# Optimization experiments

Measured on AMD Instinct MI355X. Metric: run time of the kernel, lower is better.

## Reference

```python
import jax, jax.numpy as jnp
import numpy as np

N = 50000        # nodes
E = 800000       # random edges (plus N self-loops added in setup)
DIN = 128        # input_dim
H = 128          # hidden_dim
L = 3            # num_layers
EPS = 1e-5       # BatchNorm1d eps


def _bn(x, gamma, beta):
    # BatchNorm1d in training mode: batch stats over node axis, biased variance
    m = x.mean(axis=0)
    v = jnp.mean((x - m) ** 2, axis=0)
    return (x - m) * jax.lax.rsqrt(v + EPS) * gamma + beta


def setup_inputs() -> dict:
    key = jax.random.key(0)
    ks = jax.random.split(key, 11)
    feats = jax.random.normal(ks[0], (N, DIN), dtype=jnp.float32)
    # edge list with self-loops so every node has degree >= 1 (average pooling divides by degree)
    loops = jnp.arange(N, dtype=jnp.int64)
    src = jnp.concatenate([jax.random.randint(ks[1], (E,), 0, N, dtype=jnp.int64), loops])
    dst = jnp.concatenate([jax.random.randint(ks[2], (E,), 0, N, dtype=jnp.int64), loops])
    s = 0.05
    # per-layer MLP params (num_mlp_layers=2: Linear -> BN -> ReLU -> Linear), layer 0 has DIN==H
    W1 = jax.random.normal(ks[3], (L, DIN, H), dtype=jnp.float32) * s
    b1 = jnp.zeros((L, H), jnp.float32)
    g1 = jnp.ones((L, H), jnp.float32)
    be1 = jnp.zeros((L, H), jnp.float32)
    W2 = jax.random.normal(ks[4], (L, H, H), dtype=jnp.float32) * s
    b2 = jnp.zeros((L, H), jnp.float32)
    # outer BatchNorm1d per GNN layer
    og = jnp.ones((L, H), jnp.float32)
    ob = jnp.zeros((L, H), jnp.float32)
    return {"feats": feats, "W1": W1, "b1": b1, "g1": g1, "be1": be1,
            "W2": W2, "b2": b2, "og": og, "ob": ob, "src": src, "dst": dst}


def reference(feats, W1, b1, g1, be1, W2, b2, og, ob, src, dst):
    n = feats.shape[0]
    # degree = spmm(Adj, ones) -- constant across layers
    deg = jax.ops.segment_sum(jnp.ones(src.shape, jnp.float32), dst, num_segments=n)[:, None]
    h = feats
    for l in range(L):
        # pooled = spmm(Adj, h) via edge gather + segment reduce, then 'average' normalize
        pooled = jax.ops.segment_sum(h[src], dst, num_segments=n) / deg
        # GIN-style 2-layer MLP: Linear -> BN -> ReLU -> Linear
        z = jax.nn.relu(_bn(pooled @ W1[l] + b1[l], g1[l], be1[l]))
        z = z @ W2[l] + b2[l]
        # outer BatchNorm + ReLU
        h = jax.nn.relu(_bn(z, og[l], ob[l]))
    return h
```

## Files before the change

### kernel.cpp

```cpp
#include <hip/hip_runtime.h>
#include <hip/hip_bf16.h>
#include <stdint.h>

typedef __hip_bfloat16 bf16;
typedef short bf16x8 __attribute__((ext_vector_type(8)));
typedef float f32x4 __attribute__((ext_vector_type(4)));

#define HF 128
#define EPS 1e-5f
#define BSH 9
#define BROWS 512
#define ECHUNK 8192

static __device__ __forceinline__ uint32_t pack_bf16(float a, float b) {
    union { bf16 h; unsigned short u; } ca, cb;
    ca.h = __float2bfloat16(a);
    cb.h = __float2bfloat16(b);
    return (uint32_t)ca.u | ((uint32_t)cb.u << 16);
}


__global__ __launch_bounds__(256) void k_bcount(const int* __restrict__ dst,
                                                int* __restrict__ bcnt, int ne, int nb) {
    __shared__ int h[128];
    const int tid = threadIdx.x;
    if (tid < nb) h[tid] = 0;
    __syncthreads();
    const int beg = blockIdx.x * ECHUNK;
    const int end = min(beg + ECHUNK, ne);
    for (int i = beg + tid; i < end; i += 256)
        atomicAdd(&h[dst[i] >> BSH], 1);
    __syncthreads();
    if (tid < nb && h[tid]) atomicAdd(&bcnt[tid], h[tid]);
}

__global__ __launch_bounds__(128) void k_bscan(const int* __restrict__ bcnt,
                                               int* __restrict__ bstart,
                                               int* __restrict__ gcursor,
                                               int* __restrict__ rowptr,
                                               int nb, int n, int ne) {
    if (threadIdx.x == 0) {
        int acc = 0;
        for (int b = 0; b < nb; b++) {
            bstart[b] = acc;
            gcursor[b] = acc;
            acc += bcnt[b];
        }
        bstart[nb] = acc;
        rowptr[n] = ne;
    }
}

__global__ __launch_bounds__(256) void k_bscatter(const int* __restrict__ src,
                                                  const int* __restrict__ dst,
                                                  int* __restrict__ gcursor,
                                                  int2* __restrict__ staging, int ne, int nb) {
    __shared__ int h[128], gb[128];
    const int tid = threadIdx.x;
    if (tid < nb) h[tid] = 0;
    __syncthreads();
    const int beg = blockIdx.x * ECHUNK;
    const int end = min(beg + ECHUNK, ne);
    for (int i = beg + tid; i < end; i += 256)
        atomicAdd(&h[dst[i] >> BSH], 1);
    __syncthreads();
    if (tid < nb) {
        int c = h[tid];
        gb[tid] = c ? atomicAdd(&gcursor[tid], c) : 0;
        h[tid] = 0;
    }
    __syncthreads();
    for (int i = beg + tid; i < end; i += 256) {
        int d = dst[i];
        int b = d >> BSH;
        int r = atomicAdd(&h[b], 1);
        staging[(size_t)gb[b] + r] = make_int2(src[i], d);
    }
}

__global__ __launch_bounds__(256) void k_bbuild(const int2* __restrict__ staging,
                                                const int* __restrict__ bstart,
                                                int* __restrict__ rowptr,
                                                float* __restrict__ deginv,
                                                int* __restrict__ csrsrc, int n) {
    __shared__ int hist[BROWS];
    __shared__ int scan[BROWS];
    const int b = blockIdx.x;
    const int tid = threadIdx.x;
    const int rb = b << BSH;
    const int nrows = min(BROWS, n - rb);
    const int ebeg = bstart[b], eend = bstart[b + 1];
    hist[tid] = 0; hist[tid + 256] = 0;
    __syncthreads();
    for (int i = ebeg + tid; i < eend; i += 256)
        atomicAdd(&hist[staging[i].y - rb], 1);
    __syncthreads();
    const int i0 = tid, i1 = tid + 256;
    scan[i0] = hist[i0]; scan[i1] = hist[i1];
    __syncthreads();
    for (int off = 1; off < BROWS; off <<= 1) {
        int v0 = (i0 >= off) ? scan[i0 - off] : 0;
        int v1 = (i1 >= off) ? scan[i1 - off] : 0;
        __syncthreads();
        scan[i0] += v0; scan[i1] += v1;
        __syncthreads();
    }
    for (int r = tid; r < BROWS; r += 256) {
        int c = hist[r];
        int excl = scan[r] - c;
        if (r < nrows) {
            rowptr[rb + r] = ebeg + excl;
            deginv[rb + r] = c ? 1.0f / (float)c : 0.f;
        }
        scan[r] = excl;
    }
    __syncthreads();
    for (int i = ebeg + tid; i < eend; i += 256) {
        int2 e = staging[i];
        int pos = atomicAdd(&scan[e.y - rb], 1);
        csrsrc[ebeg + pos] = e.x;
    }
}

__global__ __launch_bounds__(256) void k_wprep(const float* __restrict__ W1,
                                               const float* __restrict__ W2,
                                               bf16* __restrict__ wp) {
    const int mat = blockIdx.x >> 6;
    const int idx = ((blockIdx.x & 63) << 8) + threadIdx.x;
    const int l = mat >> 1;
    const float* Wsrc = (mat & 1) ? (W2 + l * 16384) : (W1 + l * 16384);
    const int nn = idx >> 7, k = idx & 127;
    float w = Wsrc[k * 128 + nn];
    int pos = nn * 128 + ((((k >> 3) ^ (nn & 7))) << 3) + (k & 7);
    wp[mat * 16384 + pos] = __float2bfloat16(w);
}

__global__ __launch_bounds__(256) void k_cvt(const float* __restrict__ in,
                                             uint32_t* __restrict__ out, long tot2) {
    long i = (long)blockIdx.x * 256 + threadIdx.x;
    if (i >= tot2) return;
    float2 v = ((const float2*)in)[i];
    out[i] = pack_bf16(v.x, v.y);
}

template <int AFF>
__global__ __launch_bounds__(256) void k_spmm(const uint32_t* __restrict__ hp,
                                              const int* __restrict__ rowptr,
                                              const int* __restrict__ csrsrc,
                                              const float* __restrict__ deginv,
                                              const float* __restrict__ st,
                                              const float* __restrict__ g,
                                              const float* __restrict__ be,
                                              float inv_n,
                                              uint32_t* __restrict__ pooled, int n, int np) {
    const int wid  = (int)((blockIdx.x * 256u + threadIdx.x) >> 6);
    const int lane = threadIdx.x & 63;
    if (wid >= np) return;
    uint32_t* outp = pooled + (size_t)wid * 64 + lane;
    if (wid >= n) { *outp = 0u; return; }
    float sx = 1.f, cx = 0.f, sy = 1.f, cy = 0.f;
    if (AFF) {
        const int c0 = lane * 2, c1 = c0 + 1;
        float m0 = st[c0] * inv_n, v0 = st[128 + c0] * inv_n - m0 * m0;
        sx = g[c0] * rsqrtf(v0 + EPS); cx = be[c0] - m0 * sx;
        float m1 = st[c1] * inv_n, v1 = st[128 + c1] * inv_n - m1 * m1;
        sy = g[c1] * rsqrtf(v1 + EPS); cy = be[c1] - m1 * sy;
    }
    float a0 = 0.f, a1 = 0.f;
    const int beg = rowptr[wid], end = rowptr[wid + 1];
    for (int base = beg; base < end; base += 64) {
        const int rem = end - base;
        const int cnt = rem < 64 ? rem : 64;
        const int off = lane < cnt ? lane : cnt - 1;
        const int idx = csrsrc[base + off];
        int j = 0;
        for (; j + 8 <= cnt; j += 8) {
            uint32_t p[8];
#pragma unroll
            for (int u = 0; u < 8; u++) {
                int s = __builtin_amdgcn_readlane(idx, j + u);
                p[u] = hp[(size_t)s * 64 + lane];
            }
#pragma unroll
            for (int u = 0; u < 8; u++) {
                float vx = __uint_as_float(p[u] << 16);
                float vy = __uint_as_float(p[u] & 0xFFFF0000u);
                if (AFF) {
                    vx = fmaxf(fmaf(vx, sx, cx), 0.f);
                    vy = fmaxf(fmaf(vy, sy, cy), 0.f);
                }
                a0 += vx; a1 += vy;
            }
        }
        for (; j < cnt; j++) {
            int s = __builtin_amdgcn_readlane(idx, j);
            uint32_t pk = hp[(size_t)s * 64 + lane];
            float vx = __uint_as_float(pk << 16);
            float vy = __uint_as_float(pk & 0xFFFF0000u);
            if (AFF) {
                vx = fmaxf(fmaf(vx, sx, cx), 0.f);
                vy = fmaxf(fmaf(vy, sy, cy), 0.f);
            }
            a0 += vx; a1 += vy;
        }
    }
    const float di = deginv[wid];
    *outp = pack_bf16(a0 * di, a1 * di);
}

template <int MODE, int OUTBF>
__global__ __launch_bounds__(256) void k_gemm(const bf16* __restrict__ Abf,
                                              const float* __restrict__ Af,
                                              const bf16* __restrict__ Wp,
                                              const float* __restrict__ bias,
                                              const float* __restrict__ st,
                                              const float* __restrict__ g,
                                              const float* __restrict__ be,
                                              float inv_n,
                                              float* __restrict__ Yf,
                                              bf16* __restrict__ Yb,
                                              float* __restrict__ outstats, int n) {
    __shared__ __align__(16) bf16 WT[128 * 128];
    __shared__ float sred[4][128];
    __shared__ float sred2[4][128];
    __shared__ float aff[256];
    const int tid = threadIdx.x;
    const int wave = tid >> 6, lane = tid & 63;

    {
        const char* gsrc = (const char*)Wp + wave * 1024 + lane * 16;
        char* ldst = (char*)&WT[0] + wave * 1024;
#pragma unroll
        for (int i = 0; i < 8; i++) {
            __builtin_amdgcn_global_load_lds(
                (const __attribute__((address_space(1))) uint32_t*)(gsrc + i * 4096),
                (__attribute__((address_space(3))) uint32_t*)(ldst + i * 4096),
                16, 0, 0);
        }
    }
    if (MODE == 1 && tid < 128) {
        float m = st[tid] * inv_n;
        float v = st[128 + tid] * inv_n - m * m;
        float a = g[tid] * rsqrtf(v + EPS);
        aff[tid] = a;
        aff[128 + tid] = be[tid] - m * a;
    }

    const int lrow = lane & 15, quad = lane >> 4;
    const int bx = (int)blockIdx.x * 128;
    int mb[2];
    mb[0] = bx + wave * 16;
    mb[1] = bx + 64 + wave * 16;

    bf16x8 ah[2][4], al[2][4];
    if (MODE == 0) {
#pragma unroll
        for (int rt = 0; rt < 2; rt++) {
            const bf16* arow = Abf + (size_t)(mb[rt] + lrow) * 128 + quad * 8;
#pragma unroll
            for (int kt = 0; kt < 4; kt++)
                ah[rt][kt] = *(const bf16x8*)(arow + kt * 32);
        }
    }

    __syncthreads();

    if (MODE == 1) {
#pragma unroll
        for (int rt = 0; rt < 2; rt++) {
            const float* arow = Af + (size_t)(mb[rt] + lrow) * 128 + quad * 8;
#pragma unroll
            for (int kt = 0; kt < 4; kt++) {
                short th[8], tl[8];
#pragma unroll
                for (int j = 0; j < 8; j++) {
                    int k = kt * 32 + quad * 8 + j;
                    float x = fmaxf(fmaf(arow[kt * 32 + j], aff[k], aff[128 + k]), 0.f);
                    union { bf16 b; short s; } ch, cl;
                    ch.b = __float2bfloat16(x);
                    cl.b = __float2bfloat16(x - __bfloat162float(ch.b));
                    th[j] = ch.s; tl[j] = cl.s;
                }
                ah[rt][kt] = *(bf16x8*)th;
                al[rt][kt] = *(bf16x8*)tl;
            }
        }
    }

    f32x4 acc[2][8];
#pragma unroll
    for (int rt = 0; rt < 2; rt++)
#pragma unroll
        for (int nt = 0; nt < 8; nt++) acc[rt][nt] = (f32x4){0.f, 0.f, 0.f, 0.f};

    const int sw = lrow & 7;
#pragma unroll
    for (int nt = 0; nt < 8; nt++) {
        const bf16* wbase = &WT[(nt * 16 + lrow) * 128];
#pragma unroll
        for (int kt = 0; kt < 4; kt++) {
            bf16x8 bh = *(const bf16x8*)(wbase + (((4 * kt + quad) ^ sw) << 3));
#pragma unroll
            for (int rt = 0; rt < 2; rt++) {
                acc[rt][nt] = __builtin_amdgcn_mfma_f32_16x16x32_bf16(ah[rt][kt], bh, acc[rt][nt], 0, 0, 0);
                if (MODE == 1)
                    acc[rt][nt] = __builtin_amdgcn_mfma_f32_16x16x32_bf16(al[rt][kt], bh, acc[rt][nt], 0, 0, 0);
            }
        }
    }

#pragma unroll
    for (int nt = 0; nt < 8; nt++) {
        int col = nt * 16 + lrow;
        float bv = bias[col];
        float csum = 0.f, csq = 0.f;
#pragma unroll
        for (int rt = 0; rt < 2; rt++) {
#pragma unroll
            for (int r = 0; r < 4; r++) {
                int row = mb[rt] + quad * 4 + r;
                float yv = acc[rt][nt][r] + bv;
                if (OUTBF) Yb[(size_t)row * 128 + col] = __float2bfloat16(yv);
                else       Yf[(size_t)row * 128 + col] = yv;
                if (row < n) { csum += yv; csq += yv * yv; }
            }
        }
        csum += __shfl_xor(csum, 16, 64); csum += __shfl_xor(csum, 32, 64);
        csq  += __shfl_xor(csq,  16, 64); csq  += __shfl_xor(csq,  32, 64);
        if (quad == 0) { sred[wave][col] = csum; sred2[wave][col] = csq; }
    }
    __syncthreads();
    if (tid < 128) {
        float s = sred[0][tid] + sred[1][tid] + sred[2][tid] + sred[3][tid];
        float q = sred2[0][tid] + sred2[1][tid] + sred2[2][tid] + sred2[3][tid];
        atomicAdd(&outstats[tid], s);
        atomicAdd(&outstats[128 + tid], q);
    }
}

__global__ __launch_bounds__(256) void k_bnrelu(const uint32_t* __restrict__ Z,
                                                const float* __restrict__ st,
                                                const float* __restrict__ g,
                                                const float* __restrict__ be,
                                                float inv_n,
                                                float* __restrict__ out, long tot2) {
    long i = (long)blockIdx.x * 256 + threadIdx.x;
    if (i >= tot2) return;
    int c = (int)((i * 2) & 127);
    float m0 = st[c] * inv_n,     v0 = st[128 + c] * inv_n - m0 * m0;
    float a0 = g[c] * rsqrtf(v0 + EPS),     c0 = be[c] - m0 * a0;
    float m1 = st[c + 1] * inv_n, v1 = st[129 + c] * inv_n - m1 * m1;
    float a1 = g[c + 1] * rsqrtf(v1 + EPS), c1 = be[c + 1] - m1 * a1;
    uint32_t pk = Z[i];
    float vx = __uint_as_float(pk << 16);
    float vy = __uint_as_float(pk & 0xFFFF0000u);
    float2 o;
    o.x = fmaxf(fmaf(vx, a0, c0), 0.f);
    o.y = fmaxf(fmaf(vy, a1, c1), 0.f);
    ((float2*)out)[i] = o;
}

extern "C" void kernel_launch(void* const* d_in, const int* in_sizes, int n_in,
                              void* d_out, int out_size, void* d_ws, size_t ws_size,
                              hipStream_t stream) {
    const float* feats = (const float*)d_in[0];
    const float* W1    = (const float*)d_in[1];
    const float* b1    = (const float*)d_in[2];
    const float* g1    = (const float*)d_in[3];
    const float* be1   = (const float*)d_in[4];
    const float* W2    = (const float*)d_in[5];
    const float* b2    = (const float*)d_in[6];
    const float* og    = (const float*)d_in[7];
    const float* ob    = (const float*)d_in[8];
    const int*   src   = (const int*)d_in[9];
    const int*   dst   = (const int*)d_in[10];

    const int n  = in_sizes[0] / HF;
    const int ne = in_sizes[9];
    const int np = (n + 127) & ~127;
    const int nb = (n + BROWS - 1) >> BSH;

    char* p = (char*)d_ws;
    auto alloc = [&](size_t bytes) -> char* {
        char* r = p;
        p += (bytes + 511) & ~(size_t)511;
        return r;
    };
    uint32_t* hbuf    = (uint32_t*)alloc((size_t)np * 64 * 4);
    uint32_t* pooled  = (uint32_t*)alloc((size_t)np * 64 * 4);
    float*    ybuf    = (float*)   alloc((size_t)np * HF * 4);
    uint32_t* zb      = (uint32_t*)alloc((size_t)np * 64 * 4);
    bf16*     wprep   = (bf16*)    alloc(6 * 16384 * 2);
    float*    deginv  = (float*)   alloc((size_t)n * 4);
    int*      rowptr  = (int*)     alloc((size_t)(n + 1) * 4);
    int*      csrsrc  = (int*)     alloc((size_t)ne * 4);
    int2*     staging = (int2*)    alloc((size_t)ne * 8);
    int*      bstart  = (int*)     alloc((size_t)(nb + 1) * 4);
    int*      gcursor = (int*)     alloc((size_t)nb * 4);
    char*     zone    = alloc(512 + 6 * 256 * 4);
    int*      bcnt    = (int*)zone;
    float*    stats6  = (float*)(zone + 512);

    hipMemsetAsync(zone, 0, 512 + 6 * 256 * 4, stream);

    const int ebk = (ne + ECHUNK - 1) / ECHUNK;
    k_wprep   <<<384, 256, 0, stream>>>(W1, W2, wprep);
    k_bcount  <<<ebk, 256, 0, stream>>>(dst, bcnt, ne, nb);
    k_bscan   <<<1, 128, 0, stream>>>(bcnt, bstart, gcursor, rowptr, nb, n, ne);
    k_bscatter<<<ebk, 256, 0, stream>>>(src, dst, gcursor, staging, ne, nb);
    k_bbuild  <<<nb, 256, 0, stream>>>(staging, bstart, rowptr, deginv, csrsrc, n);

    const long tot2  = (long)n * (HF / 2);
    const int bnb    = (int)((tot2 + 255) / 256);
    const int spmmb  = np / 4;
    const int gemmb  = np / 128;
    const float inv_n = 1.0f / (float)n;

    k_cvt<<<bnb, 256, 0, stream>>>(feats, hbuf, tot2);

    for (int l = 0; l < 3; l++) {
        float* sY = stats6 + (2 * l) * 256;
        float* sZ = stats6 + (2 * l + 1) * 256;
        if (l == 0)
            k_spmm<0><<<spmmb, 256, 0, stream>>>(hbuf, rowptr, csrsrc, deginv,
                                                 nullptr, nullptr, nullptr, inv_n,
                                                 pooled, n, np);
        else
            k_spmm<1><<<spmmb, 256, 0, stream>>>(zb, rowptr, csrsrc, deginv,
                                                 stats6 + (2 * (l - 1) + 1) * 256,
                                                 og + (l - 1) * HF, ob + (l - 1) * HF, inv_n,
                                                 pooled, n, np);
        k_gemm<0, 0><<<gemmb, 256, 0, stream>>>((const bf16*)pooled, nullptr,
                                                wprep + (size_t)(2 * l) * 16384,
                                                b1 + l * HF,
                                                nullptr, nullptr, nullptr, inv_n,
                                                ybuf, nullptr, sY, n);
        k_gemm<1, 1><<<gemmb, 256, 0, stream>>>(nullptr, ybuf,
                                                wprep + (size_t)(2 * l + 1) * 16384,
                                                b2 + l * HF,
                                                sY, g1 + l * HF, be1 + l * HF, inv_n,
                                                nullptr, (bf16*)zb, sZ, n);
    }
    k_bnrelu<<<bnb, 256, 0, stream>>>(zb, stats6 + 5 * 256, og + 2 * HF, ob + 2 * HF,
                                      inv_n, (float*)d_out, tot2);
}
```

Before: 395.0 us.

## Use fixed-capacity edge buckets, merge prep kernels, and bank BN stat atomics

```diff
diff --git a/kernel.cpp b/kernel.cpp
--- a/kernel.cpp
+++ b/kernel.cpp
@@ -10,7 +10,9 @@
 #define EPS 1e-5f
 #define BSH 9
 #define BROWS 512
+#define BCAP 16384
 #define ECHUNK 8192
+#define SBANKS 8
 
 static __device__ __forceinline__ uint32_t pack_bf16(float a, float b) {
     union { bf16 h; unsigned short u; } ca, cb;
@@ -19,37 +21,13 @@
     return (uint32_t)ca.u | ((uint32_t)cb.u << 16);
 }
 
-
-__global__ __launch_bounds__(256) void k_bcount(const int* __restrict__ dst,
-                                                int* __restrict__ bcnt, int ne, int nb) {
-    __shared__ int h[128];
-    const int tid = threadIdx.x;
-    if (tid < nb) h[tid] = 0;
-    __syncthreads();
-    const int beg = blockIdx.x * ECHUNK;
-    const int end = min(beg + ECHUNK, ne);
-    for (int i = beg + tid; i < end; i += 256)
-        atomicAdd(&h[dst[i] >> BSH], 1);
-    __syncthreads();
-    if (tid < nb && h[tid]) atomicAdd(&bcnt[tid], h[tid]);
-}
-
-__global__ __launch_bounds__(128) void k_bscan(const int* __restrict__ bcnt,
-                                               int* __restrict__ bstart,
-                                               int* __restrict__ gcursor,
-                                               int* __restrict__ rowptr,
-                                               int nb, int n, int ne) {
-    if (threadIdx.x == 0) {
-        int acc = 0;
-        for (int b = 0; b < nb; b++) {
-            bstart[b] = acc;
-            gcursor[b] = acc;
-            acc += bcnt[b];
-        }
-        bstart[nb] = acc;
-        rowptr[n] = ne;
-    }
-}
+static __device__ __forceinline__ float sum8(const float* __restrict__ st, int idx) {
+    float s = 0.f;
+#pragma unroll
+    for (int b = 0; b < SBANKS; b++) s += st[b * 256 + idx];
+    return s;
+}
+
 
 __global__ __launch_bounds__(256) void k_bscatter(const int* __restrict__ src,
                                                   const int* __restrict__ dst,
@@ -74,13 +52,14 @@
         int d = dst[i];
         int b = d >> BSH;
         int r = atomicAdd(&h[b], 1);
-        staging[(size_t)gb[b] + r] = make_int2(src[i], d);
+        staging[(size_t)b * BCAP + gb[b] + r] = make_int2(src[i], d);
     }
 }
 
 __global__ __launch_bounds__(256) void k_bbuild(const int2* __restrict__ staging,
-                                                const int* __restrict__ bstart,
-                                                int* __restrict__ rowptr,
+                                                const int* __restrict__ gcursor,
+                                                int* __restrict__ rowbeg,
+                                                int* __restrict__ rowend,
                                                 float* __restrict__ deginv,
                                                 int* __restrict__ csrsrc, int n) {
     __shared__ int hist[BROWS];
@@ -89,11 +68,12 @@
     const int tid = threadIdx.x;
     const int rb = b << BSH;
     const int nrows = min(BROWS, n - rb);
-    const int ebeg = bstart[b], eend = bstart[b + 1];
+    const int base = b * BCAP;
+    const int cnt = gcursor[b];
     hist[tid] = 0; hist[tid + 256] = 0;
     __syncthreads();
-    for (int i = ebeg + tid; i < eend; i += 256)
-        atomicAdd(&hist[staging[i].y - rb], 1);
+    for (int i = tid; i < cnt; i += 256)
+        atomicAdd(&hist[staging[base + i].y - rb], 1);
     __syncthreads();
     const int i0 = tid, i1 = tid + 256;
     scan[i0] = hist[i0]; scan[i1] = hist[i1];
@@ -109,49 +89,54 @@
         int c = hist[r];
         int excl = scan[r] - c;
         if (r < nrows) {
-            rowptr[rb + r] = ebeg + excl;
+            rowbeg[rb + r] = base + excl;
+            rowend[rb + r] = base + excl + c;
             deginv[rb + r] = c ? 1.0f / (float)c : 0.f;
         }
         scan[r] = excl;
     }
     __syncthreads();
-    for (int i = ebeg + tid; i < eend; i += 256) {
-        int2 e = staging[i];
+    for (int i = tid; i < cnt; i += 256) {
+        int2 e = staging[base + i];
         int pos = atomicAdd(&scan[e.y - rb], 1);
-        csrsrc[ebeg + pos] = e.x;
-    }
-}
-
-__global__ __launch_bounds__(256) void k_wprep(const float* __restrict__ W1,
-                                               const float* __restrict__ W2,
-                                               bf16* __restrict__ wp) {
-    const int mat = blockIdx.x >> 6;
-    const int idx = ((blockIdx.x & 63) << 8) + threadIdx.x;
-    const int l = mat >> 1;
-    const float* Wsrc = (mat & 1) ? (W2 + l * 16384) : (W1 + l * 16384);
-    const int nn = idx >> 7, k = idx & 127;
-    float w = Wsrc[k * 128 + nn];
-    int pos = nn * 128 + ((((k >> 3) ^ (nn & 7))) << 3) + (k & 7);
-    wp[mat * 16384 + pos] = __float2bfloat16(w);
-}
-
-__global__ __launch_bounds__(256) void k_cvt(const float* __restrict__ in,
-                                             uint32_t* __restrict__ out, long tot2) {
-    long i = (long)blockIdx.x * 256 + threadIdx.x;
-    if (i >= tot2) return;
-    float2 v = ((const float2*)in)[i];
-    out[i] = pack_bf16(v.x, v.y);
+        csrsrc[base + pos] = e.x;
+    }
+}
+
+__global__ __launch_bounds__(256) void k_prep(const float* __restrict__ W1,
+                                              const float* __restrict__ W2,
+                                              bf16* __restrict__ wp,
+                                              const float* __restrict__ feats,
+                                              uint32_t* __restrict__ hbuf, long tot2) {
+    const int bid = (int)blockIdx.x;
+    if (bid < 384) {
+        const int mat = bid >> 6;
+        const int idx = ((bid & 63) << 8) + (int)threadIdx.x;
+        const int l = mat >> 1;
+        const float* Wsrc = (mat & 1) ? (W2 + l * 16384) : (W1 + l * 16384);
+        const int nn = idx >> 7, k = idx & 127;
+        float w = Wsrc[k * 128 + nn];
+        int pos = nn * 128 + ((((k >> 3) ^ (nn & 7))) << 3) + (k & 7);
+        wp[mat * 16384 + pos] = __float2bfloat16(w);
+    } else {
+        long i = (long)(bid - 384) * 256 + threadIdx.x;
+        if (i < tot2) {
+            float2 v = ((const float2*)feats)[i];
+            hbuf[i] = pack_bf16(v.x, v.y);
+        }
+    }
 }
 
 template <int AFF>
 __global__ __launch_bounds__(256) void k_spmm(const uint32_t* __restrict__ hp,
-                                              const int* __restrict__ rowptr,
-                                              const int* __restrict__ csrsrc,
+                                              const int* __restrict__ rowbeg,
+                                              const int* __restrict__ rowend,
                                               const float* __restrict__ deginv,
                                               const float* __restrict__ st,
                                               const float* __restrict__ g,
                                               const float* __restrict__ be,
                                               float inv_n,
+                                              const int* __restrict__ csrsrc,
                                               uint32_t* __restrict__ pooled, int n, int np) {
     const int wid  = (int)((blockIdx.x * 256u + threadIdx.x) >> 6);
     const int lane = threadIdx.x & 63;
@@ -161,13 +146,13 @@
     float sx = 1.f, cx = 0.f, sy = 1.f, cy = 0.f;
     if (AFF) {
         const int c0 = lane * 2, c1 = c0 + 1;
-        float m0 = st[c0] * inv_n, v0 = st[128 + c0] * inv_n - m0 * m0;
+        float m0 = sum8(st, c0) * inv_n, v0 = sum8(st, 128 + c0) * inv_n - m0 * m0;
         sx = g[c0] * rsqrtf(v0 + EPS); cx = be[c0] - m0 * sx;
-        float m1 = st[c1] * inv_n, v1 = st[128 + c1] * inv_n - m1 * m1;
+        float m1 = sum8(st, c1) * inv_n, v1 = sum8(st, 128 + c1) * inv_n - m1 * m1;
         sy = g[c1] * rsqrtf(v1 + EPS); cy = be[c1] - m1 * sy;
     }
     float a0 = 0.f, a1 = 0.f;
-    const int beg = rowptr[wid], end = rowptr[wid + 1];
+    const int beg = rowbeg[wid], end = rowend[wid];
     for (int base = beg; base < end; base += 64) {
         const int rem = end - base;
         const int cnt = rem < 64 ? rem : 64;
@@ -239,8 +224,8 @@
         }
     }
     if (MODE == 1 && tid < 128) {
-        float m = st[tid] * inv_n;
-        float v = st[128 + tid] * inv_n - m * m;
+        float m = sum8(st, tid) * inv_n;
+        float v = sum8(st, 128 + tid) * inv_n - m * m;
         float a = g[tid] * rsqrtf(v + EPS);
         aff[tid] = a;
         aff[128 + tid] = be[tid] - m * a;
@@ -333,8 +318,9 @@
     if (tid < 128) {
         float s = sred[0][tid] + sred[1][tid] + sred[2][tid] + sred[3][tid];
         float q = sred2[0][tid] + sred2[1][tid] + sred2[2][tid] + sred2[3][tid];
-        atomicAdd(&outstats[tid], s);
-        atomicAdd(&outstats[128 + tid], q);
+        const int bank = (int)(blockIdx.x & (SBANKS - 1));
+        atomicAdd(&outstats[bank * 256 + tid], s);
+        atomicAdd(&outstats[bank * 256 + 128 + tid], q);
     }
 }
 
@@ -347,9 +333,9 @@
     long i = (long)blockIdx.x * 256 + threadIdx.x;
     if (i >= tot2) return;
     int c = (int)((i * 2) & 127);
-    float m0 = st[c] * inv_n,     v0 = st[128 + c] * inv_n - m0 * m0;
+    float m0 = sum8(st, c) * inv_n,     v0 = sum8(st, 128 + c) * inv_n - m0 * m0;
     float a0 = g[c] * rsqrtf(v0 + EPS),     c0 = be[c] - m0 * a0;
-    float m1 = st[c + 1] * inv_n, v1 = st[129 + c] * inv_n - m1 * m1;
+    float m1 = sum8(st, c + 1) * inv_n, v1 = sum8(st, 129 + c) * inv_n - m1 * m1;
     float a1 = g[c + 1] * rsqrtf(v1 + EPS), c1 = be[c + 1] - m1 * a1;
     uint32_t pk = Z[i];
     float vx = __uint_as_float(pk << 16);
@@ -392,44 +378,40 @@
     uint32_t* zb      = (uint32_t*)alloc((size_t)np * 64 * 4);
     bf16*     wprep   = (bf16*)    alloc(6 * 16384 * 2);
     float*    deginv  = (float*)   alloc((size_t)n * 4);
-    int*      rowptr  = (int*)     alloc((size_t)(n + 1) * 4);
-    int*      csrsrc  = (int*)     alloc((size_t)ne * 4);
-    int2*     staging = (int2*)    alloc((size_t)ne * 8);
-    int*      bstart  = (int*)     alloc((size_t)(nb + 1) * 4);
-    int*      gcursor = (int*)     alloc((size_t)nb * 4);
-    char*     zone    = alloc(512 + 6 * 256 * 4);
-    int*      bcnt    = (int*)zone;
+    int*      rowbeg  = (int*)     alloc((size_t)n * 4);
+    int*      rowend  = (int*)     alloc((size_t)n * 4);
+    int*      csrsrc  = (int*)     alloc((size_t)nb * BCAP * 4);
+    int2*     staging = (int2*)    alloc((size_t)nb * BCAP * 8);
+    char*     zone    = alloc(512 + 6 * SBANKS * 256 * 4);
+    int*      gcursor = (int*)zone;
     float*    stats6  = (float*)(zone + 512);
 
-    hipMemsetAsync(zone, 0, 512 + 6 * 256 * 4, stream);
-
-    const int ebk = (ne + ECHUNK - 1) / ECHUNK;
-    k_wprep   <<<384, 256, 0, stream>>>(W1, W2, wprep);
-    k_bcount  <<<ebk, 256, 0, stream>>>(dst, bcnt, ne, nb);
-    k_bscan   <<<1, 128, 0, stream>>>(bcnt, bstart, gcursor, rowptr, nb, n, ne);
-    k_bscatter<<<ebk, 256, 0, stream>>>(src, dst, gcursor, staging, ne, nb);
-    k_bbuild  <<<nb, 256, 0, stream>>>(staging, bstart, rowptr, deginv, csrsrc, n);
+    hipMemsetAsync(zone, 0, 512 + 6 * SBANKS * 256 * 4, stream);
 
     const long tot2  = (long)n * (HF / 2);
     const int bnb    = (int)((tot2 + 255) / 256);
     const int spmmb  = np / 4;
     const int gemmb  = np / 128;
     const float inv_n = 1.0f / (float)n;
-
-    k_cvt<<<bnb, 256, 0, stream>>>(feats, hbuf, tot2);
+    const int ebk = (ne + ECHUNK - 1) / ECHUNK;
+    const int SL = SBANKS * 256;
+
+    k_prep    <<<384 + bnb, 256, 0, stream>>>(W1, W2, wprep, feats, hbuf, tot2);
+    k_bscatter<<<ebk, 256, 0, stream>>>(src, dst, gcursor, staging, ne, nb);
+    k_bbuild  <<<nb, 256, 0, stream>>>(staging, gcursor, rowbeg, rowend, deginv, csrsrc, n);
 
     for (int l = 0; l < 3; l++) {
-        float* sY = stats6 + (2 * l) * 256;
-        float* sZ = stats6 + (2 * l + 1) * 256;
+        float* sY = stats6 + (2 * l) * SL;
+        float* sZ = stats6 + (2 * l + 1) * SL;
         if (l == 0)
-            k_spmm<0><<<spmmb, 256, 0, stream>>>(hbuf, rowptr, csrsrc, deginv,
+            k_spmm<0><<<spmmb, 256, 0, stream>>>(hbuf, rowbeg, rowend, deginv,
                                                  nullptr, nullptr, nullptr, inv_n,
-                                                 pooled, n, np);
+                                                 csrsrc, pooled, n, np);
         else
-            k_spmm<1><<<spmmb, 256, 0, stream>>>(zb, rowptr, csrsrc, deginv,
-                                                 stats6 + (2 * (l - 1) + 1) * 256,
+            k_spmm<1><<<spmmb, 256, 0, stream>>>(zb, rowbeg, rowend, deginv,
+                                                 stats6 + (2 * (l - 1) + 1) * SL,
                                                  og + (l - 1) * HF, ob + (l - 1) * HF, inv_n,
-                                                 pooled, n, np);
+                                                 csrsrc, pooled, n, np);
         k_gemm<0, 0><<<gemmb, 256, 0, stream>>>((const bf16*)pooled, nullptr,
                                                 wprep + (size_t)(2 * l) * 16384,
                                                 b1 + l * HF,
@@ -441,6 +423,6 @@
                                                 sY, g1 + l * HF, be1 + l * HF, inv_n,
                                                 nullptr, (bf16*)zb, sZ, n);
     }
-    k_bnrelu<<<bnb, 256, 0, stream>>>(zb, stats6 + 5 * 256, og + 2 * HF, ob + 2 * HF,
+    k_bnrelu<<<bnb, 256, 0, stream>>>(zb, stats6 + 5 * SL, og + 2 * HF, ob + 2 * HF,
                                       inv_n, (float*)d_out, tot2);
 }
```

After: 384.4 us. -2.7%, faster.
